# Performance work log

Hardware: AMD Instinct MI355X
Metric: run time of the kernel (lower is better)

The kernel has to match this reference:

```python
import jax, jax.numpy as jnp
import numpy as np

B, P, G, H, W = 4, 24, 24, 512, 512
IOU_THRESH = 0.5
SMOOTH = 1.0
LOG_CLAMP = -100.0  # torch F.binary_cross_entropy clamps log terms at -100


def _pairwise_iou(pb, gb):
    # pb: [B,P,4], gb: [B,G,4]; boxes are (y1,x1,y2,x2), normalized
    a = pb[:, :, None, :]  # [B,P,1,4]
    b = gb[:, None, :, :]  # [B,1,G,4]
    area_a = (a[..., 2] - a[..., 0]) * (a[..., 3] - a[..., 1])
    area_b = (b[..., 2] - b[..., 0]) * (b[..., 3] - b[..., 1])
    int_h = jnp.maximum(jnp.minimum(a[..., 2], b[..., 2]) - jnp.maximum(a[..., 0], b[..., 0]), 0.0)
    int_w = jnp.maximum(jnp.minimum(a[..., 3], b[..., 3]) - jnp.maximum(a[..., 1], b[..., 1]), 0.0)
    inter = int_h * int_w
    union = area_a + area_b - inter
    return jnp.where(union == 0.0, 0.0, inter / jnp.where(union == 0.0, 1.0, union))  # [B,P,G]


def _seg_loss(pred_masks, pred_boxes, gt_boxes, gt_masks, pred_valid, gt_valid):
    # IoU matching (argmax over gt, keep if max IoU >= 0.5)
    iou = _pairwise_iou(pred_boxes, gt_boxes)                      # [B,P,G]
    iou = jnp.where(gt_valid[:, None, :], iou, -1.0)
    max_iou = jnp.max(iou, axis=-1)                                # [B,P]
    gt_idx = jnp.argmax(iou, axis=-1)                              # [B,P]
    keep = (max_iou >= IOU_THRESH) & pred_valid                    # [B,P]

    # integer crop coords, matching np.round (half-to-even) + clamping of the source
    y1 = jnp.maximum(0, jnp.round(pred_boxes[..., 0] * H).astype(jnp.int32))
    x1 = jnp.maximum(0, jnp.round(pred_boxes[..., 1] * W).astype(jnp.int32))
    y2 = jnp.minimum(jnp.round(pred_boxes[..., 2] * H).astype(jnp.int32), H - 1)
    x2 = jnp.minimum(jnp.round(pred_boxes[..., 3] * W).astype(jnp.int32), W - 1)

    rows = jnp.arange(H)[None, None, :, None]                      # [1,1,H,1]
    cols = jnp.arange(W)[None, None, None, :]                      # [1,1,1,W]
    region = ((rows >= y1[..., None, None]) & (rows <= y2[..., None, None]) &
              (cols >= x1[..., None, None]) & (cols <= x2[..., None, None]))
    rf = region.astype(pred_masks.dtype)                           # [B,P,H,W]

    # gather matched gt masks: [B,P,H,W]
    t = jnp.take_along_axis(gt_masks, gt_idx[:, :, None, None], axis=1)
    p = pred_masks

    # BCE over the crop region (mean over crop pixels)
    logp = jnp.clip(jnp.log(p), LOG_CLAMP)
    log1mp = jnp.clip(jnp.log1p(-p), LOG_CLAMP)
    bce_px = -(t * logp + (1.0 - t) * log1mp) * rf
    cnt = jnp.sum(rf, axis=(2, 3))                                 # [B,P]
    bce = jnp.sum(bce_px, axis=(2, 3)) / jnp.maximum(cnt, 1.0)

    # Dice over the crop region
    pr = p * rf
    tr = t * rf
    inter = jnp.sum(pr * tr, axis=(2, 3))
    dice = 1.0 - (2.0 * inter + SMOOTH) / (jnp.sum(pr, axis=(2, 3)) + jnp.sum(tr, axis=(2, 3)) + SMOOTH)

    loss_obj = bce + dice                                          # [B,P]
    n_obj = jnp.sum(keep.astype(jnp.float32))
    total = jnp.sum(jnp.where(keep, loss_obj, 0.0))
    return total / jnp.maximum(n_obj, 1.0)


def setup_inputs() -> dict:
    key = jax.random.key(0)
    k0, k1, k2, k3, k4, k5, k6 = jax.random.split(key, 7)
    # valid gt boxes: size in [0.1, 0.5], fully inside the unit square
    sz = jax.random.uniform(k0, (B, G, 2), minval=0.1, maxval=0.5)
    tl = jax.random.uniform(k1, (B, G, 2)) * (1.0 - sz)
    gt_boxes = jnp.concatenate([tl, tl + sz], axis=-1).astype(jnp.float32)  # (y1,x1,y2,x2)
    # predictions = jittered gt boxes so IoU>=0.5 matches occur
    raw = gt_boxes + 0.02 * jax.random.normal(k2, (B, P, 4))
    pred_boxes = jnp.clip(jnp.concatenate([jnp.minimum(raw[..., :2], raw[..., 2:]),
                                           jnp.maximum(raw[..., :2], raw[..., 2:])], axis=-1), 0.0, 1.0)
    pred_boxes = pred_boxes.astype(jnp.float32)
    pred_masks = jax.random.uniform(k3, (B, P, H, W), minval=1e-4, maxval=1.0 - 1e-4, dtype=jnp.float32)
    gt_masks = (jax.random.uniform(k4, (B, G, H, W)) > 0.5).astype(jnp.float32)
    pred_valid = jax.random.uniform(k5, (B, P)) > 0.2
    gt_valid = jax.random.uniform(k6, (B, G)) > 0.2
    return {"pred_masks": pred_masks, "pred_boxes": pred_boxes, "gt_boxes": gt_boxes,
            "gt_masks": gt_masks, "pred_valid": pred_valid, "gt_valid": gt_valid}


def reference(pred_masks, pred_boxes, gt_boxes, gt_masks, pred_valid, gt_valid):
    return _seg_loss(pred_masks, pred_boxes, gt_boxes, gt_masks, pred_valid, gt_valid)
```

## Files before the change

### kernel.cpp

```cpp
#include <hip/hip_runtime.h>
#include <math.h>

#define Bn 4
#define Pn 24
#define Gn 24
#define Hd 512
#define Wd 512
#define NOBJ (Bn * Pn)
#define SPLIT 16
#define IOU_THRESH 0.5f

#define AUX_OFF (NOBJ * SPLIT * 4)

__device__ __forceinline__ void match_obj(const float* __restrict__ pred_boxes,
                                          const float* __restrict__ gt_boxes,
                                          const int* __restrict__ pred_valid,
                                          const int* __restrict__ gt_valid,
                                          int obj, int& keep, int& gidx,
                                          int& y1, int& x1, int& y2, int& x2) {
    int b = obj / Pn;
    const float* pb = pred_boxes + (size_t)obj * 4;
    float a0 = pb[0], a1 = pb[1], a2 = pb[2], a3 = pb[3];
    float area_a = (a2 - a0) * (a3 - a1);
    float best = -1.0f;
    gidx = 0;
    #pragma unroll
    for (int g = 0; g < Gn; ++g) {
        const float* gb = gt_boxes + ((size_t)b * Gn + g) * 4;
        float b0 = gb[0], b1 = gb[1], b2 = gb[2], b3 = gb[3];
        float area_b = (b2 - b0) * (b3 - b1);
        float ih = fmaxf(fminf(a2, b2) - fmaxf(a0, b0), 0.0f);
        float iw = fmaxf(fminf(a3, b3) - fmaxf(a1, b1), 0.0f);
        float inter = ih * iw;
        float uni = area_a + area_b - inter;
        float iou = (uni == 0.0f) ? 0.0f : inter / uni;
        if (gt_valid[b * Gn + g] == 0) iou = -1.0f;
        if (iou > best) { best = iou; gidx = g; }
    }
    keep = (best >= IOU_THRESH) && (pred_valid[obj] != 0);
    y1 = max(0, (int)rintf(a0 * (float)Hd));
    x1 = max(0, (int)rintf(a1 * (float)Wd));
    y2 = min((int)rintf(a2 * (float)Hd), Hd - 1);
    x2 = min((int)rintf(a3 * (float)Wd), Wd - 1);
}

__global__ __launch_bounds__(256) void region_kernel(
    const float* __restrict__ pred_masks, const float* __restrict__ gt_masks,
    const float* __restrict__ pred_boxes, const float* __restrict__ gt_boxes,
    const int* __restrict__ pred_valid, const int* __restrict__ gt_valid,
    float* __restrict__ acc, float* __restrict__ aux) {
    int obj = blockIdx.x;
    int part = blockIdx.y;

    int keep, gidx, y1, x1, y2, x2;
    match_obj(pred_boxes, gt_boxes, pred_valid, gt_valid, obj, keep, gidx, y1, x1, y2, x2);

    float v0 = 0.0f, v1 = 0.0f, v2 = 0.0f, v3 = 0.0f;
    if (keep && y2 >= y1 && x2 >= x1) {
        int Wr = x2 - x1 + 1;
        int Hr = y2 - y1 + 1;
        int x1a = x1 & ~3;
        int W4 = (x2 >> 2) - (x1 >> 2) + 1;
        int N4 = Hr * W4;
        int idx = part * 256 + (int)threadIdx.x;
        if (idx < N4) {
            const float* pm = pred_masks + (size_t)obj * Hd * Wd + x1a;
            const float* gm = gt_masks + ((size_t)(obj / Pn) * Gn + gidx) * Hd * Wd + x1a;
            const int step = SPLIT * 256;
            int r = idx / W4;
            int c = idx - r * W4;
            int dr = step / W4;
            int dc = step - dr * W4;
            int rel0 = x1a - x1;
            while (true) {
                int off = (y1 + r) * Wd + (c << 2);
                float4 p4 = *reinterpret_cast<const float4*>(pm + off);
                float4 q4 = *reinterpret_cast<const float4*>(gm + off);
                int rel = rel0 + (c << 2);
                bool m0 = (unsigned)(rel + 0) < (unsigned)Wr;
                bool m1 = (unsigned)(rel + 1) < (unsigned)Wr;
                bool m2 = (unsigned)(rel + 2) < (unsigned)Wr;
                bool m3 = (unsigned)(rel + 3) < (unsigned)Wr;
                float p0 = m0 ? p4.x : 0.0f, q0 = m0 ? q4.x : 0.0f;
                float p1 = m1 ? p4.y : 0.0f, q1 = m1 ? q4.y : 0.0f;
                float p2 = m2 ? p4.z : 0.0f, q2 = m2 ? q4.z : 0.0f;
                float p3 = m3 ? p4.w : 0.0f, q3 = m3 ? q4.w : 0.0f;
                float a0 = (q0 > 0.5f) ? p0 : 1.0f - p0;
                float a1 = (q1 > 0.5f) ? p1 : 1.0f - p1;
                float a2 = (q2 > 0.5f) ? p2 : 1.0f - p2;
                float a3 = (q3 > 0.5f) ? p3 : 1.0f - p3;
                v0 -= __logf((a0 * a1) * (a2 * a3));
                v1 = fmaf(p0, q0, fmaf(p1, q1, fmaf(p2, q2, fmaf(p3, q3, v1))));
                v2 += (p0 + p1) + (p2 + p3);
                v3 += (q0 + q1) + (q2 + q3);
                idx += step;
                if (idx >= N4) break;
                c += dc; r += dr;
                if (c >= W4) { c -= W4; ++r; }
            }
        }
    }

    for (int o = 32; o > 0; o >>= 1) {
        v0 += __shfl_down(v0, o, 64);
        v1 += __shfl_down(v1, o, 64);
        v2 += __shfl_down(v2, o, 64);
        v3 += __shfl_down(v3, o, 64);
    }
    __shared__ float red[4][4];
    int lane = threadIdx.x & 63, w = threadIdx.x >> 6;
    if (lane == 0) { red[w][0] = v0; red[w][1] = v1; red[w][2] = v2; red[w][3] = v3; }
    __syncthreads();
    if (threadIdx.x < 4) {
        float sfin = red[0][threadIdx.x] + red[1][threadIdx.x] +
                     red[2][threadIdx.x] + red[3][threadIdx.x];
        acc[((size_t)obj * SPLIT + part) * 4 + threadIdx.x] = sfin;
    } else if (part == 0 && threadIdx.x == 4) {
        float cnt = (y2 >= y1 && x2 >= x1)
                      ? (float)((y2 - y1 + 1) * (x2 - x1 + 1)) : 0.0f;
        aux[obj * 2 + 0] = keep ? 1.0f : 0.0f;
        aux[obj * 2 + 1] = cnt;
    }
}

__global__ __launch_bounds__(128) void finalize_kernel(
    const float* __restrict__ acc, const float* __restrict__ aux,
    float* __restrict__ out) {
    int i = threadIdx.x;
    float loss = 0.0f, nk = 0.0f;
    if (i < NOBJ) {
        float keepf = aux[i * 2 + 0];
        float cnt = aux[i * 2 + 1];
        if (keepf > 0.5f) {
            nk = 1.0f;
            const float4* a = reinterpret_cast<const float4*>(acc) + (size_t)i * SPLIT;
            float s0 = 0.0f, s1 = 0.0f, s2 = 0.0f, s3 = 0.0f;
            #pragma unroll
            for (int p = 0; p < SPLIT; ++p) {
                float4 v = a[p];
                s0 += v.x; s1 += v.y; s2 += v.z; s3 += v.w;
            }
            float bce = s0 / fmaxf(cnt, 1.0f);
            float dice = 1.0f - (2.0f * s1 + 1.0f) / (s2 + s3 + 1.0f);
            loss = bce + dice;
        }
    }
    float v0 = loss, v1 = nk;
    for (int o = 32; o > 0; o >>= 1) {
        v0 += __shfl_down(v0, o, 64);
        v1 += __shfl_down(v1, o, 64);
    }
    __shared__ float red[2][2];
    if ((threadIdx.x & 63) == 0) { red[threadIdx.x >> 6][0] = v0; red[threadIdx.x >> 6][1] = v1; }
    __syncthreads();
    if (threadIdx.x == 0) {
        float total = red[0][0] + red[1][0];
        float nobj = red[0][1] + red[1][1];
        out[0] = total / fmaxf(nobj, 1.0f);
    }
}

extern "C" void kernel_launch(void* const* d_in, const int* in_sizes, int n_in,
                              void* d_out, int out_size, void* d_ws, size_t ws_size,
                              hipStream_t stream) {
    const float* pred_masks = (const float*)d_in[0];
    const float* pred_boxes = (const float*)d_in[1];
    const float* gt_boxes   = (const float*)d_in[2];
    const float* gt_masks   = (const float*)d_in[3];
    const int*   pred_valid = (const int*)d_in[4];
    const int*   gt_valid   = (const int*)d_in[5];
    float* out = (float*)d_out;
    float* acc = (float*)d_ws;
    float* aux = acc + AUX_OFF;

    region_kernel<<<dim3(NOBJ, SPLIT), 256, 0, stream>>>(
        pred_masks, gt_masks, pred_boxes, gt_boxes, pred_valid, gt_valid, acc, aux);
    finalize_kernel<<<1, 128, 0, stream>>>(acc, aux, out);
}
```

Baseline: 19.27 us.

## Prefetch pred masks before IoU matching and software-pipeline two loads per thread

Issues the first pred-mask loads before the 24-way IoU matching loop so memory latency overlaps the matching arithmetic. The main loop now handles two float4 groups per iteration and prefetches the next pair ahead of processing them. SPLIT is halved, so there are fewer blocks and each thread does more work. The cost is higher register pressure and fewer blocks to spread across the GPU. Pred-mask loads are also spent on objects that turn out not to be kept.

After: 15.96 us. 17.2% less time.

```diff
diff --git a/kernel.cpp b/kernel.cpp
--- a/kernel.cpp
+++ b/kernel.cpp
@@ -7,41 +7,30 @@
 #define Hd 512
 #define Wd 512
 #define NOBJ (Bn * Pn)
-#define SPLIT 16
+#define SPLIT 8
+#define STEP (SPLIT * 256)
 #define IOU_THRESH 0.5f
 
 #define AUX_OFF (NOBJ * SPLIT * 4)
 
-__device__ __forceinline__ void match_obj(const float* __restrict__ pred_boxes,
-                                          const float* __restrict__ gt_boxes,
-                                          const int* __restrict__ pred_valid,
-                                          const int* __restrict__ gt_valid,
-                                          int obj, int& keep, int& gidx,
-                                          int& y1, int& x1, int& y2, int& x2) {
-    int b = obj / Pn;
-    const float* pb = pred_boxes + (size_t)obj * 4;
-    float a0 = pb[0], a1 = pb[1], a2 = pb[2], a3 = pb[3];
-    float area_a = (a2 - a0) * (a3 - a1);
-    float best = -1.0f;
-    gidx = 0;
-    #pragma unroll
-    for (int g = 0; g < Gn; ++g) {
-        const float* gb = gt_boxes + ((size_t)b * Gn + g) * 4;
-        float b0 = gb[0], b1 = gb[1], b2 = gb[2], b3 = gb[3];
-        float area_b = (b2 - b0) * (b3 - b1);
-        float ih = fmaxf(fminf(a2, b2) - fmaxf(a0, b0), 0.0f);
-        float iw = fmaxf(fminf(a3, b3) - fmaxf(a1, b1), 0.0f);
-        float inter = ih * iw;
-        float uni = area_a + area_b - inter;
-        float iou = (uni == 0.0f) ? 0.0f : inter / uni;
-        if (gt_valid[b * Gn + g] == 0) iou = -1.0f;
-        if (iou > best) { best = iou; gidx = g; }
-    }
-    keep = (best >= IOU_THRESH) && (pred_valid[obj] != 0);
-    y1 = max(0, (int)rintf(a0 * (float)Hd));
-    x1 = max(0, (int)rintf(a1 * (float)Wd));
-    y2 = min((int)rintf(a2 * (float)Hd), Hd - 1);
-    x2 = min((int)rintf(a3 * (float)Wd), Wd - 1);
+__device__ __forceinline__ void proc_group(float4 p4, float4 q4, int rel, int Wr,
+                                           float& v0, float& v1, float& v2, float& v3) {
+    bool m0 = (unsigned)(rel + 0) < (unsigned)Wr;
+    bool m1 = (unsigned)(rel + 1) < (unsigned)Wr;
+    bool m2 = (unsigned)(rel + 2) < (unsigned)Wr;
+    bool m3 = (unsigned)(rel + 3) < (unsigned)Wr;
+    float p0 = m0 ? p4.x : 0.0f, q0 = m0 ? q4.x : 0.0f;
+    float p1 = m1 ? p4.y : 0.0f, q1 = m1 ? q4.y : 0.0f;
+    float p2 = m2 ? p4.z : 0.0f, q2 = m2 ? q4.z : 0.0f;
+    float p3 = m3 ? p4.w : 0.0f, q3 = m3 ? q4.w : 0.0f;
+    float a0 = (q0 > 0.5f) ? p0 : 1.0f - p0;
+    float a1 = (q1 > 0.5f) ? p1 : 1.0f - p1;
+    float a2 = (q2 > 0.5f) ? p2 : 1.0f - p2;
+    float a3 = (q3 > 0.5f) ? p3 : 1.0f - p3;
+    v0 -= __logf((a0 * a1) * (a2 * a3));
+    v1 = fmaf(p0, q0, fmaf(p1, q1, fmaf(p2, q2, fmaf(p3, q3, v1))));
+    v2 += (p0 + p1) + (p2 + p3);
+    v3 += (q0 + q1) + (q2 + q3);
 }
 
 __global__ __launch_bounds__(256) void region_kernel(
@@ -51,53 +40,102 @@
     float* __restrict__ acc, float* __restrict__ aux) {
     int obj = blockIdx.x;
     int part = blockIdx.y;
-
-    int keep, gidx, y1, x1, y2, x2;
-    match_obj(pred_boxes, gt_boxes, pred_valid, gt_valid, obj, keep, gidx, y1, x1, y2, x2);
-
-    float v0 = 0.0f, v1 = 0.0f, v2 = 0.0f, v3 = 0.0f;
-    if (keep && y2 >= y1 && x2 >= x1) {
-        int Wr = x2 - x1 + 1;
+    int b = obj / Pn;
+
+    const float* pbp = pred_boxes + (size_t)obj * 4;
+    float A0 = pbp[0], A1 = pbp[1], A2 = pbp[2], A3 = pbp[3];
+    int y1 = max(0, (int)rintf(A0 * (float)Hd));
+    int x1 = max(0, (int)rintf(A1 * (float)Wd));
+    int y2 = min((int)rintf(A2 * (float)Hd), Hd - 1);
+    int x2 = min((int)rintf(A3 * (float)Wd), Wd - 1);
+    bool rect_ok = (y2 >= y1 && x2 >= x1);
+
+    int Wr = 0, W4 = 0, N4 = 0, rel0 = 0;
+    const float* pm = pred_masks + (size_t)obj * Hd * Wd;
+    float4 pA, qA, pB, qB;
+    int idxA = 0, idxB = 0, rA = 0, cA = 0, rB = 0, cB = 0;
+    bool hasA = false, hasB = false;
+    if (rect_ok) {
+        Wr = x2 - x1 + 1;
         int Hr = y2 - y1 + 1;
         int x1a = x1 & ~3;
-        int W4 = (x2 >> 2) - (x1 >> 2) + 1;
-        int N4 = Hr * W4;
-        int idx = part * 256 + (int)threadIdx.x;
-        if (idx < N4) {
-            const float* pm = pred_masks + (size_t)obj * Hd * Wd + x1a;
-            const float* gm = gt_masks + ((size_t)(obj / Pn) * Gn + gidx) * Hd * Wd + x1a;
-            const int step = SPLIT * 256;
-            int r = idx / W4;
-            int c = idx - r * W4;
-            int dr = step / W4;
-            int dc = step - dr * W4;
-            int rel0 = x1a - x1;
-            while (true) {
-                int off = (y1 + r) * Wd + (c << 2);
-                float4 p4 = *reinterpret_cast<const float4*>(pm + off);
-                float4 q4 = *reinterpret_cast<const float4*>(gm + off);
-                int rel = rel0 + (c << 2);
-                bool m0 = (unsigned)(rel + 0) < (unsigned)Wr;
-                bool m1 = (unsigned)(rel + 1) < (unsigned)Wr;
-                bool m2 = (unsigned)(rel + 2) < (unsigned)Wr;
-                bool m3 = (unsigned)(rel + 3) < (unsigned)Wr;
-                float p0 = m0 ? p4.x : 0.0f, q0 = m0 ? q4.x : 0.0f;
-                float p1 = m1 ? p4.y : 0.0f, q1 = m1 ? q4.y : 0.0f;
-                float p2 = m2 ? p4.z : 0.0f, q2 = m2 ? q4.z : 0.0f;
-                float p3 = m3 ? p4.w : 0.0f, q3 = m3 ? q4.w : 0.0f;
-                float a0 = (q0 > 0.5f) ? p0 : 1.0f - p0;
-                float a1 = (q1 > 0.5f) ? p1 : 1.0f - p1;
-                float a2 = (q2 > 0.5f) ? p2 : 1.0f - p2;
-                float a3 = (q3 > 0.5f) ? p3 : 1.0f - p3;
-                v0 -= __logf((a0 * a1) * (a2 * a3));
-                v1 = fmaf(p0, q0, fmaf(p1, q1, fmaf(p2, q2, fmaf(p3, q3, v1))));
-                v2 += (p0 + p1) + (p2 + p3);
-                v3 += (q0 + q1) + (q2 + q3);
-                idx += step;
-                if (idx >= N4) break;
-                c += dc; r += dr;
-                if (c >= W4) { c -= W4; ++r; }
+        W4 = (x2 >> 2) - (x1 >> 2) + 1;
+        N4 = Hr * W4;
+        rel0 = x1a - x1;
+        pm += x1a;
+        idxA = part * 256 + (int)threadIdx.x;
+        if (idxA < N4) {
+            hasA = true;
+            rA = idxA / W4;
+            cA = idxA - rA * W4;
+            pA = *reinterpret_cast<const float4*>(pm + (y1 + rA) * Wd + (cA << 2));
+            idxB = idxA + STEP;
+            if (idxB < N4) {
+                hasB = true;
+                int dS = STEP / W4, cS = STEP - (STEP / W4) * W4;
+                rB = rA + dS; cB = cA + cS;
+                if (cB >= W4) { cB -= W4; ++rB; }
+                pB = *reinterpret_cast<const float4*>(pm + (y1 + rB) * Wd + (cB << 2));
             }
+        }
+    }
+
+    float area_a = (A2 - A0) * (A3 - A1);
+    float best = -1.0f;
+    int gidx = 0;
+    #pragma unroll
+    for (int g = 0; g < Gn; ++g) {
+        const float* gb = gt_boxes + ((size_t)b * Gn + g) * 4;
+        float b0 = gb[0], b1 = gb[1], b2 = gb[2], b3 = gb[3];
+        float area_b = (b2 - b0) * (b3 - b1);
+        float ih = fmaxf(fminf(A2, b2) - fmaxf(A0, b0), 0.0f);
+        float iw = fmaxf(fminf(A3, b3) - fmaxf(A1, b1), 0.0f);
+        float inter = ih * iw;
+        float uni = area_a + area_b - inter;
+        float iou = (uni == 0.0f) ? 0.0f : inter / uni;
+        if (gt_valid[b * Gn + g] == 0) iou = -1.0f;
+        if (iou > best) { best = iou; gidx = g; }
+    }
+    int keep = (best >= IOU_THRESH) && (pred_valid[obj] != 0);
+
+    float v0 = 0.0f, v1 = 0.0f, v2 = 0.0f, v3 = 0.0f;
+    if (keep && hasA) {
+        const float* gm = gt_masks + ((size_t)b * Gn + gidx) * Hd * Wd + ((x1 & ~3));
+        qA = *reinterpret_cast<const float4*>(gm + (y1 + rA) * Wd + (cA << 2));
+        if (hasB)
+            qB = *reinterpret_cast<const float4*>(gm + (y1 + rB) * Wd + (cB << 2));
+        const int S2 = 2 * STEP;
+        int dr2 = S2 / W4, dc2 = S2 - (S2 / W4) * W4;
+        while (true) {
+            int idxA2 = idxA + S2;
+            bool hasA2 = idxA2 < N4;
+            bool hasB2 = false;
+            float4 pA2, qA2, pB2, qB2;
+            int rA2 = rA, cA2 = cA, rB2 = rB, cB2 = cB;
+            if (hasA2) {
+                cA2 = cA + dc2; rA2 = rA + dr2;
+                if (cA2 >= W4) { cA2 -= W4; ++rA2; }
+                int off = (y1 + rA2) * Wd + (cA2 << 2);
+                pA2 = *reinterpret_cast<const float4*>(pm + off);
+                qA2 = *reinterpret_cast<const float4*>(gm + off);
+                int idxB2 = idxB + S2;
+                if (idxB2 < N4) {
+                    hasB2 = true;
+                    cB2 = cB + dc2; rB2 = rB + dr2;
+                    if (cB2 >= W4) { cB2 -= W4; ++rB2; }
+                    int offb = (y1 + rB2) * Wd + (cB2 << 2);
+                    pB2 = *reinterpret_cast<const float4*>(pm + offb);
+                    qB2 = *reinterpret_cast<const float4*>(gm + offb);
+                }
+            }
+            proc_group(pA, qA, rel0 + (cA << 2), Wr, v0, v1, v2, v3);
+            if (hasB)
+                proc_group(pB, qB, rel0 + (cB << 2), Wr, v0, v1, v2, v3);
+            if (!hasA2) break;
+            idxA = idxA2; idxB = idxB + S2;
+            rA = rA2; cA = cA2; rB = rB2; cB = cB2;
+            pA = pA2; qA = qA2; pB = pB2; qB = qB2;
+            hasB = hasB2;
         }
     }
 
@@ -116,8 +154,7 @@
                      red[2][threadIdx.x] + red[3][threadIdx.x];
         acc[((size_t)obj * SPLIT + part) * 4 + threadIdx.x] = sfin;
     } else if (part == 0 && threadIdx.x == 4) {
-        float cnt = (y2 >= y1 && x2 >= x1)
-                      ? (float)((y2 - y1 + 1) * (x2 - x1 + 1)) : 0.0f;
+        float cnt = rect_ok ? (float)((y2 - y1 + 1) * (x2 - x1 + 1)) : 0.0f;
         aux[obj * 2 + 0] = keep ? 1.0f : 0.0f;
         aux[obj * 2 + 1] = cnt;
     }
```
